# Performance work log

Hardware: AMD Instinct MI355X
Metric: run time of the kernel (lower is better)

The kernel has to match this reference:

```python
import jax, jax.numpy as jnp
import numpy as np
import math

IN_DIM = 512
PARAM_DIM = 512
OUT_DIM = 2048
GROUPS = 4
COMPRESS = 4
PLANES = OUT_DIM // COMPRESS          # 512
GROUP_PLANES = PLANES // GROUPS       # 128
ATTN_SCALE = PLANES ** (-0.5)         # note: full planes, as in the source
N, L = 16, 1024
M = L  # required by sv.reshape(N, planes, L)


def equal_linear(x, w, b, in_dim):
    # EqualLinear: F.linear(x, w * (1/sqrt(in_dim)) * lr_mul, bias * lr_mul), lr_mul=1
    scale = 1.0 / math.sqrt(in_dim)
    return jnp.einsum('nlc,oc->nlo', x, w * scale) + b


def setup_inputs() -> dict:
    key = jax.random.key(0)
    ks = jax.random.split(key, 8)
    return {
        'attention': jax.random.normal(ks[0], (N, L, IN_DIM), dtype=jnp.float32),
        'op_param': jax.random.normal(ks[1], (N, M, PARAM_DIM), dtype=jnp.float32),
        'q_w': jax.random.normal(ks[2], (PLANES, PARAM_DIM), dtype=jnp.float32),
        'q_b': jnp.zeros((PLANES,), dtype=jnp.float32),
        'k_w': jax.random.normal(ks[3], (PLANES, IN_DIM), dtype=jnp.float32),
        'k_b': jnp.zeros((PLANES,), dtype=jnp.float32),
        'v_w': jax.random.normal(ks[4], (PLANES, IN_DIM), dtype=jnp.float32),
        'v_b': jnp.zeros((PLANES,), dtype=jnp.float32),
        'proj_w': jax.random.normal(ks[5], (OUT_DIM, PLANES), dtype=jnp.float32),
        'proj_b': jnp.zeros((OUT_DIM,), dtype=jnp.float32),
    }


def reference(attention, op_param, q_w, q_b, k_w, k_b, v_w, v_b, proj_w, proj_b):
    n, l, _ = attention.shape
    m = op_param.shape[1]
    # q/k/v: (N, T, planes) -> (N, groups, group_planes, T)
    q = equal_linear(op_param, q_w, q_b, PARAM_DIM).reshape(n, m, GROUPS, GROUP_PLANES).transpose(0, 2, 3, 1)
    k = equal_linear(attention, k_w, k_b, IN_DIM).reshape(n, l, GROUPS, GROUP_PLANES).transpose(0, 2, 3, 1)
    v = equal_linear(attention, v_w, v_b, IN_DIM).reshape(n, l, GROUPS, GROUP_PLANES).transpose(0, 2, 3, 1)
    # scores: (N, groups, M, L)
    qk = jnp.einsum('ngdm,ngdl->ngml', q, k) * ATTN_SCALE
    sim = jax.nn.softmax(qk, axis=3)
    # sv: (N, groups, group_planes, M)
    sv = jnp.einsum('ngml,ngdl->ngdm', sim, v)
    # (N, planes, L) -> (N, L, planes); valid because M == L
    stacked = sv.reshape(n, PLANES, l).transpose(0, 2, 1)
    out = equal_linear(stacked, proj_w, proj_b, PLANES)
    return out
```

## Files before the change

### kernel.cpp

```cpp
#include <hip/hip_runtime.h>
#include <hip/hip_bf16.h>

#define NB 16
#define TT 1024
#define CC 512
#define PP 512
#define GG 4
#define DD 128
#define OO 2048

#define SCL 0.04419417382415922f

typedef __attribute__((ext_vector_type(8))) short short8;
typedef __attribute__((ext_vector_type(4))) float floatx4;
#define MFMA(a, b, c) __builtin_amdgcn_mfma_f32_16x16x32_bf16((a), (b), (c), 0, 0, 0)

static __device__ __forceinline__ float bf2f(unsigned short u) {
  union { unsigned int i; float f; } v; v.i = ((unsigned int)u) << 16; return v.f;
}
static __device__ __forceinline__ unsigned short f2bf(float f) {
  union { float f; unsigned int i; } v; v.f = f;
  unsigned int r = (v.i + 0x7fffu + ((v.i >> 16) & 1u)) >> 16;
  return (unsigned short)r;
}
static __device__ __forceinline__ ushort4 pack4(float4 v) {
  ushort4 o; o.x = f2bf(v.x); o.y = f2bf(v.y); o.z = f2bf(v.z); o.w = f2bf(v.w); return o;
}

template <int VLAY>
__global__ __launch_bounds__(256) void k_proj(
    const float* __restrict__ x, const float* __restrict__ w,
    const float* __restrict__ b, unsigned short* __restrict__ y) {
  __shared__ unsigned short Aw[128][32];
  __shared__ unsigned short Xw[128][32];
  const int n  = blockIdx.z;
  const int p0 = blockIdx.y * 128;
  const int t0 = blockIdx.x * 128;
  const int tid  = threadIdx.x;
  const int wave = tid >> 6, lane = tid & 63;
  const int l15  = lane & 15, quad = lane >> 4;
  const int wm = (wave >> 1) * 64, wn = (wave & 1) * 64;
  const int srow = tid >> 3, scol = (tid & 7) * 4;
  const float* xn = x + (size_t)n * TT * CC;
  floatx4 acc[4][4] = {};

  for (int k0 = 0; k0 < CC; k0 += 32) {
    float4 aw[4], ax[4];
#pragma unroll
    for (int q = 0; q < 4; ++q) {
      aw[q] = *reinterpret_cast<const float4*>(w  + (size_t)(p0 + srow + q * 32) * CC + k0 + scol);
      ax[q] = *reinterpret_cast<const float4*>(xn + (size_t)(t0 + srow + q * 32) * CC + k0 + scol);
    }
    __syncthreads();
#pragma unroll
    for (int q = 0; q < 4; ++q) {
      *reinterpret_cast<ushort4*>(&Aw[srow + q * 32][scol]) = pack4(aw[q]);
      *reinterpret_cast<ushort4*>(&Xw[srow + q * 32][scol]) = pack4(ax[q]);
    }
    __syncthreads();
    short8 af[4], bx[4];
#pragma unroll
    for (int mt = 0; mt < 4; ++mt)
      af[mt] = *reinterpret_cast<const short8*>(&Aw[wm + mt * 16 + l15][quad * 8]);
#pragma unroll
    for (int nt = 0; nt < 4; ++nt)
      bx[nt] = *reinterpret_cast<const short8*>(&Xw[wn + nt * 16 + l15][quad * 8]);
#pragma unroll
    for (int mt = 0; mt < 4; ++mt)
#pragma unroll
      for (int nt = 0; nt < 4; ++nt)
        acc[mt][nt] = MFMA(af[mt], bx[nt], acc[mt][nt]);
  }

#pragma unroll
  for (int mt = 0; mt < 4; ++mt) {
    const int pb = p0 + wm + mt * 16 + quad * 4;
    const float4 bias = *reinterpret_cast<const float4*>(b + pb);
    const float bb[4] = {bias.x, bias.y, bias.z, bias.w};
#pragma unroll
    for (int nt = 0; nt < 4; ++nt) {
      const int tc = t0 + wn + nt * 16 + l15;
      if (VLAY == 0) {
        ushort4 o;
        o.x = f2bf(acc[mt][nt][0] * SCL + bb[0]);
        o.y = f2bf(acc[mt][nt][1] * SCL + bb[1]);
        o.z = f2bf(acc[mt][nt][2] * SCL + bb[2]);
        o.w = f2bf(acc[mt][nt][3] * SCL + bb[3]);
        *reinterpret_cast<ushort4*>(y + ((size_t)n * TT + tc) * PP + pb) = o;
      } else {
#pragma unroll
        for (int r = 0; r < 4; ++r)
          y[((size_t)n * PP + pb + r) * TT + tc] = f2bf(acc[mt][nt][r] * SCL + bb[r]);
      }
    }
  }
}

__global__ __launch_bounds__(256) void k_attn(
    const unsigned short* __restrict__ Q,
    const unsigned short* __restrict__ K,
    const unsigned short* __restrict__ V,
    unsigned short* __restrict__ SV) {
  __shared__ unsigned short Sc[32][1032];
  __shared__ float rowinv[32];
  const int m0 = blockIdx.x * 32;
  const int g  = blockIdx.y;
  const int n  = blockIdx.z;
  const int tid  = threadIdx.x;
  const int wave = tid >> 6, lane = tid & 63;
  const int l15  = lane & 15, quad = lane >> 4;

  const unsigned short* Qn = Q + (size_t)n * TT * PP;
  const unsigned short* Kn = K + (size_t)n * TT * PP;
  const unsigned short* Vn = V + ((size_t)n * PP + g * DD) * TT;

  short8 aq[2][4];
#pragma unroll
  for (int mt = 0; mt < 2; ++mt)
#pragma unroll
    for (int ds = 0; ds < 4; ++ds)
      aq[mt][ds] = *reinterpret_cast<const short8*>(
          Qn + (size_t)(m0 + mt * 16 + l15) * PP + g * DD + ds * 32 + quad * 8);

#pragma unroll
  for (int pass = 0; pass < 4; ++pass) {
    short8 bk[4][4];
#pragma unroll
    for (int ds = 0; ds < 4; ++ds)
#pragma unroll
      for (int j = 0; j < 4; ++j)
        bk[ds][j] = *reinterpret_cast<const short8*>(
            Kn + (size_t)(pass * 256 + (wave * 4 + j) * 16 + l15) * PP +
            g * DD + ds * 32 + quad * 8);
    floatx4 acc[2][4] = {};
#pragma unroll
    for (int ds = 0; ds < 4; ++ds)
#pragma unroll
      for (int j = 0; j < 4; ++j) {
        acc[0][j] = MFMA(aq[0][ds], bk[ds][j], acc[0][j]);
        acc[1][j] = MFMA(aq[1][ds], bk[ds][j], acc[1][j]);
      }
#pragma unroll
    for (int mt = 0; mt < 2; ++mt)
#pragma unroll
      for (int j = 0; j < 4; ++j) {
        const int lc = pass * 256 + (wave * 4 + j) * 16 + l15;
#pragma unroll
        for (int r = 0; r < 4; ++r)
          Sc[mt * 16 + quad * 4 + r][lc] = f2bf(acc[mt][j][r] * SCL);
      }
  }
  __syncthreads();

  {
    const int mi = tid >> 3;
    const int j  = tid & 7;
    unsigned short* row = &Sc[mi][0];
    float mx = -1e30f;
#pragma unroll
    for (int i = 0; i < 16; ++i) {
      short8 u = *reinterpret_cast<const short8*>(&row[(i * 8 + j) * 8]);
      float a0 = fmaxf(bf2f((unsigned short)u[0]), bf2f((unsigned short)u[1]));
      float a1 = fmaxf(bf2f((unsigned short)u[2]), bf2f((unsigned short)u[3]));
      float a2 = fmaxf(bf2f((unsigned short)u[4]), bf2f((unsigned short)u[5]));
      float a3 = fmaxf(bf2f((unsigned short)u[6]), bf2f((unsigned short)u[7]));
      mx = fmaxf(mx, fmaxf(fmaxf(a0, a1), fmaxf(a2, a3)));
    }
#pragma unroll
    for (int off = 4; off; off >>= 1) mx = fmaxf(mx, __shfl_xor(mx, off, 8));
    float sum = 0.f;
#pragma unroll
    for (int i = 0; i < 16; ++i) {
      short8 u = *reinterpret_cast<short8*>(&row[(i * 8 + j) * 8]);
      short8 o;
      float s0 = 0.f, s1 = 0.f;
#pragma unroll
      for (int e = 0; e < 8; e += 2) {
        float e0 = __expf(bf2f((unsigned short)u[e])     - mx);
        float e1 = __expf(bf2f((unsigned short)u[e + 1]) - mx);
        s0 += e0; s1 += e1;
        o[e]     = (short)f2bf(e0);
        o[e + 1] = (short)f2bf(e1);
      }
      sum += s0 + s1;
      *reinterpret_cast<short8*>(&row[(i * 8 + j) * 8]) = o;
    }
#pragma unroll
    for (int off = 4; off; off >>= 1) sum += __shfl_xor(sum, off, 8);
    if (j == 0) rowinv[mi] = 1.f / sum;
  }
  __syncthreads();

  floatx4 av[2][2] = {};
#pragma unroll 4
  for (int ls = 0; ls < 32; ++ls) {
    short8 va[2], bp[2];
#pragma unroll
    for (int a = 0; a < 2; ++a)
      va[a] = *reinterpret_cast<const short8*>(
          Vn + (size_t)(wave * 32 + a * 16 + l15) * TT + ls * 32 + quad * 8);
#pragma unroll
    for (int mt = 0; mt < 2; ++mt)
      bp[mt] = *reinterpret_cast<const short8*>(&Sc[mt * 16 + l15][ls * 32 + quad * 8]);
#pragma unroll
    for (int a = 0; a < 2; ++a)
#pragma unroll
      for (int mt = 0; mt < 2; ++mt)
        av[a][mt] = MFMA(va[a], bp[mt], av[a][mt]);
  }
#pragma unroll
  for (int a = 0; a < 2; ++a) {
    const int pb = g * DD + wave * 32 + a * 16 + quad * 4;
#pragma unroll
    for (int mt = 0; mt < 2; ++mt) {
      const float inv = rowinv[mt * 16 + l15];
      ushort4 o;
      o.x = f2bf(av[a][mt][0] * inv);
      o.y = f2bf(av[a][mt][1] * inv);
      o.z = f2bf(av[a][mt][2] * inv);
      o.w = f2bf(av[a][mt][3] * inv);
      *reinterpret_cast<ushort4*>(
          SV + ((size_t)n * TT + m0 + mt * 16 + l15) * PP + pb) = o;
    }
  }
}

__global__ __launch_bounds__(256) void k_out(
    const unsigned short* __restrict__ SVp, const float* __restrict__ w,
    const float* __restrict__ b, float* __restrict__ out) {
  __shared__ unsigned short Wt[128][32];
  __shared__ unsigned short St[128][32];
  const int n  = blockIdx.z;
  const int o0 = blockIdx.y * 128;
  const int t0 = blockIdx.x * 128;
  const int tid  = threadIdx.x;
  const int wave = tid >> 6, lane = tid & 63;
  const int l15  = lane & 15, quad = lane >> 4;
  const int wm = (wave >> 1) * 64, wn = (wave & 1) * 64;
  const int srow = tid >> 3, scol = (tid & 7) * 4;
  const unsigned short* SVn = SVp + (size_t)n * TT * PP;
  floatx4 acc[4][4] = {};

  for (int k0 = 0; k0 < PP; k0 += 32) {
    float4 awf[4];
    ushort4 us[4];
#pragma unroll
    for (int q = 0; q < 4; ++q) {
      awf[q] = *reinterpret_cast<const float4*>(w + (size_t)(o0 + srow + q * 32) * PP + k0 + scol);
      us[q]  = *reinterpret_cast<const ushort4*>(SVn + (size_t)(t0 + srow + q * 32) * PP + k0 + scol);
    }
    __syncthreads();
#pragma unroll
    for (int q = 0; q < 4; ++q) {
      *reinterpret_cast<ushort4*>(&Wt[srow + q * 32][scol]) = pack4(awf[q]);
      *reinterpret_cast<ushort4*>(&St[srow + q * 32][scol]) = us[q];
    }
    __syncthreads();
    short8 af[4], bs[4];
#pragma unroll
    for (int mt = 0; mt < 4; ++mt)
      af[mt] = *reinterpret_cast<const short8*>(&Wt[wm + mt * 16 + l15][quad * 8]);
#pragma unroll
    for (int nt = 0; nt < 4; ++nt)
      bs[nt] = *reinterpret_cast<const short8*>(&St[wn + nt * 16 + l15][quad * 8]);
#pragma unroll
    for (int mt = 0; mt < 4; ++mt)
#pragma unroll
      for (int nt = 0; nt < 4; ++nt)
        acc[mt][nt] = MFMA(af[mt], bs[nt], acc[mt][nt]);
  }

#pragma unroll
  for (int mt = 0; mt < 4; ++mt) {
    const int ob = o0 + wm + mt * 16 + quad * 4;
    const float4 bias = *reinterpret_cast<const float4*>(b + ob);
    const float bb[4] = {bias.x, bias.y, bias.z, bias.w};
#pragma unroll
    for (int nt = 0; nt < 4; ++nt) {
      const int tc = t0 + wn + nt * 16 + l15;
      float4 o;
      o.x = acc[mt][nt][0] * SCL + bb[0];
      o.y = acc[mt][nt][1] * SCL + bb[1];
      o.z = acc[mt][nt][2] * SCL + bb[2];
      o.w = acc[mt][nt][3] * SCL + bb[3];
      *reinterpret_cast<float4*>(out + ((size_t)n * TT + tc) * OO + ob) = o;
    }
  }
}

extern "C" void kernel_launch(void* const* d_in, const int* in_sizes, int n_in,
                              void* d_out, int out_size, void* d_ws, size_t ws_size,
                              hipStream_t stream) {
  (void)in_sizes; (void)n_in; (void)out_size; (void)ws_size;
  const float* attention = (const float*)d_in[0];
  const float* op_param  = (const float*)d_in[1];
  const float* q_w = (const float*)d_in[2];
  const float* q_b = (const float*)d_in[3];
  const float* k_w = (const float*)d_in[4];
  const float* k_b = (const float*)d_in[5];
  const float* v_w = (const float*)d_in[6];
  const float* v_b = (const float*)d_in[7];
  const float* proj_w = (const float*)d_in[8];
  const float* proj_b = (const float*)d_in[9];
  float* out = (float*)d_out;

  const size_t NPT = (size_t)NB * PP * TT;
  unsigned short* scratch = (unsigned short*)d_out;
  unsigned short* Qw  = scratch;
  unsigned short* Kw  = scratch + NPT;
  unsigned short* Vw  = scratch + 2 * NPT;
  unsigned short* SVw = (unsigned short*)d_ws;

  dim3 blk(256);
  dim3 gp(TT / 128, PP / 128, NB);
  k_proj<0><<<gp, blk, 0, stream>>>(op_param,  q_w, q_b, Qw);
  k_proj<0><<<gp, blk, 0, stream>>>(attention, k_w, k_b, Kw);
  k_proj<1><<<gp, blk, 0, stream>>>(attention, v_w, v_b, Vw);
  k_attn<<<dim3(TT / 32, GG, NB), blk, 0, stream>>>(Qw, Kw, Vw, SVw);
  k_out<<<dim3(TT / 128, OO / 128, NB), blk, 0, stream>>>(SVw, proj_w, proj_b, out);
}
```

Before: 450.4 us.

## Fuse K and V projections into one kernel and swizzle attention block order

```diff
diff --git a/kernel.cpp b/kernel.cpp
--- a/kernel.cpp
+++ b/kernel.cpp
@@ -19,9 +19,8 @@
   union { unsigned int i; float f; } v; v.i = ((unsigned int)u) << 16; return v.f;
 }
 static __device__ __forceinline__ unsigned short f2bf(float f) {
-  union { float f; unsigned int i; } v; v.f = f;
-  unsigned int r = (v.i + 0x7fffu + ((v.i >> 16) & 1u)) >> 16;
-  return (unsigned short)r;
+  __hip_bfloat16 h = __float2bfloat16(f);
+  return *reinterpret_cast<unsigned short*>(&h);
 }
 static __device__ __forceinline__ ushort4 pack4(float4 v) {
   ushort4 o; o.x = f2bf(v.x); o.y = f2bf(v.y); o.z = f2bf(v.z); o.w = f2bf(v.w); return o;
@@ -96,6 +95,83 @@
   }
 }
 
+__global__ __launch_bounds__(256) void k_projkv(
+    const float* __restrict__ x,
+    const float* __restrict__ kw, const float* __restrict__ kb,
+    const float* __restrict__ vw, const float* __restrict__ vb,
+    unsigned short* __restrict__ yk, unsigned short* __restrict__ yv) {
+  __shared__ unsigned short Ak[128][32];
+  __shared__ unsigned short Av[128][32];
+  __shared__ unsigned short Xw[128][32];
+  const int n  = blockIdx.z;
+  const int p0 = blockIdx.y * 128;
+  const int t0 = blockIdx.x * 128;
+  const int tid  = threadIdx.x;
+  const int wave = tid >> 6, lane = tid & 63;
+  const int l15  = lane & 15, quad = lane >> 4;
+  const int wm = (wave >> 1) * 64, wn = (wave & 1) * 64;
+  const int srow = tid >> 3, scol = (tid & 7) * 4;
+  const float* xn = x + (size_t)n * TT * CC;
+  floatx4 ack[4][4] = {};
+  floatx4 acv[4][4] = {};
+
+  for (int k0 = 0; k0 < CC; k0 += 32) {
+    float4 a1[4], a2[4], ax[4];
+#pragma unroll
+    for (int q = 0; q < 4; ++q) {
+      a1[q] = *reinterpret_cast<const float4*>(kw + (size_t)(p0 + srow + q * 32) * CC + k0 + scol);
+      a2[q] = *reinterpret_cast<const float4*>(vw + (size_t)(p0 + srow + q * 32) * CC + k0 + scol);
+      ax[q] = *reinterpret_cast<const float4*>(xn + (size_t)(t0 + srow + q * 32) * CC + k0 + scol);
+    }
+    __syncthreads();
+#pragma unroll
+    for (int q = 0; q < 4; ++q) {
+      *reinterpret_cast<ushort4*>(&Ak[srow + q * 32][scol]) = pack4(a1[q]);
+      *reinterpret_cast<ushort4*>(&Av[srow + q * 32][scol]) = pack4(a2[q]);
+      *reinterpret_cast<ushort4*>(&Xw[srow + q * 32][scol]) = pack4(ax[q]);
+    }
+    __syncthreads();
+    short8 afk[4], afv[4], bx[4];
+#pragma unroll
+    for (int mt = 0; mt < 4; ++mt) {
+      afk[mt] = *reinterpret_cast<const short8*>(&Ak[wm + mt * 16 + l15][quad * 8]);
+      afv[mt] = *reinterpret_cast<const short8*>(&Av[wm + mt * 16 + l15][quad * 8]);
+    }
+#pragma unroll
+    for (int nt = 0; nt < 4; ++nt)
+      bx[nt] = *reinterpret_cast<const short8*>(&Xw[wn + nt * 16 + l15][quad * 8]);
+#pragma unroll
+    for (int mt = 0; mt < 4; ++mt)
+#pragma unroll
+      for (int nt = 0; nt < 4; ++nt) {
+        ack[mt][nt] = MFMA(afk[mt], bx[nt], ack[mt][nt]);
+        acv[mt][nt] = MFMA(afv[mt], bx[nt], acv[mt][nt]);
+      }
+  }
+
+#pragma unroll
+  for (int mt = 0; mt < 4; ++mt) {
+    const int pb = p0 + wm + mt * 16 + quad * 4;
+    const float4 biask = *reinterpret_cast<const float4*>(kb + pb);
+    const float4 biasv = *reinterpret_cast<const float4*>(vb + pb);
+    const float bk_[4] = {biask.x, biask.y, biask.z, biask.w};
+    const float bv_[4] = {biasv.x, biasv.y, biasv.z, biasv.w};
+#pragma unroll
+    for (int nt = 0; nt < 4; ++nt) {
+      const int tc = t0 + wn + nt * 16 + l15;
+      ushort4 o;
+      o.x = f2bf(ack[mt][nt][0] * SCL + bk_[0]);
+      o.y = f2bf(ack[mt][nt][1] * SCL + bk_[1]);
+      o.z = f2bf(ack[mt][nt][2] * SCL + bk_[2]);
+      o.w = f2bf(ack[mt][nt][3] * SCL + bk_[3]);
+      *reinterpret_cast<ushort4*>(yk + ((size_t)n * TT + tc) * PP + pb) = o;
+#pragma unroll
+      for (int r = 0; r < 4; ++r)
+        yv[((size_t)n * PP + pb + r) * TT + tc] = f2bf(acv[mt][nt][r] * SCL + bv_[r]);
+    }
+  }
+}
+
 __global__ __launch_bounds__(256) void k_attn(
     const unsigned short* __restrict__ Q,
     const unsigned short* __restrict__ K,
@@ -103,9 +179,11 @@
     unsigned short* __restrict__ SV) {
   __shared__ unsigned short Sc[32][1032];
   __shared__ float rowinv[32];
-  const int m0 = blockIdx.x * 32;
-  const int g  = blockIdx.y;
-  const int n  = blockIdx.z;
+  const int lin = blockIdx.x;
+  const int wu  = (lin >> 3) | ((lin & 7) << 8);
+  const int m0 = (wu & 31) * 32;
+  const int g  = (wu >> 5) & 3;
+  const int n  = wu >> 7;
   const int tid  = threadIdx.x;
   const int wave = tid >> 6, lane = tid & 63;
   const int l15  = lane & 15, quad = lane >> 4;
@@ -313,9 +391,8 @@
 
   dim3 blk(256);
   dim3 gp(TT / 128, PP / 128, NB);
-  k_proj<0><<<gp, blk, 0, stream>>>(op_param,  q_w, q_b, Qw);
-  k_proj<0><<<gp, blk, 0, stream>>>(attention, k_w, k_b, Kw);
-  k_proj<1><<<gp, blk, 0, stream>>>(attention, v_w, v_b, Vw);
-  k_attn<<<dim3(TT / 32, GG, NB), blk, 0, stream>>>(Qw, Kw, Vw, SVw);
+  k_proj<0><<<gp, blk, 0, stream>>>(op_param, q_w, q_b, Qw);
+  k_projkv<<<gp, blk, 0, stream>>>(attention, k_w, k_b, v_w, v_b, Kw, Vw);
+  k_attn<<<dim3(2048), blk, 0, stream>>>(Qw, Kw, Vw, SVw);
   k_out<<<dim3(TT / 128, OO / 128, NB), blk, 0, stream>>>(SVw, proj_w, proj_b, out);
 }
```

Result: slower. 469.4 us (+4.2%).
